# Performance work log

Measured on AMD Instinct MI355X. Metric: run time of the kernel, lower is better.

## Reference

```python
import jax, jax.numpy as jnp
import numpy as np

K = 6

def _diag_indices(H, W):
    # stable argsort of anti-diagonal index i+j over row-major flattening
    i = np.arange(H)[:, None]
    j = np.arange(W)[None, :]
    order = np.argsort((i + j).ravel(), kind='stable')
    return order, np.argsort(order, kind='stable')

def _selective_scan(u, delta, A, Bs, Cs, D, delta_bias):
    # u, delta: (B,K,D,L); A: (K,D,N); Bs,Cs: (B,K,N,L); D,delta_bias: (K,D)
    delta = jax.nn.softplus(delta + delta_bias[None, :, :, None])
    dA = jnp.exp(jnp.einsum('bkdl,kdn->lbkdn', delta, A))          # (L,B,K,D,N)
    dBu = jnp.einsum('bkdl,bknl,bkdl->lbkdn', delta, Bs, u)         # (L,B,K,D,N)
    Cl = jnp.moveaxis(Cs, -1, 0)                                    # (L,B,K,N)
    x0 = jnp.zeros(dA.shape[1:], dA.dtype)
    def step(x, inp):
        dA_t, dBu_t, C_t = inp
        x = dA_t * x + dBu_t
        y = jnp.einsum('bkdn,bkn->bkd', x, C_t)
        return x, y
    _, ys = jax.lax.scan(step, x0, (dA, dBu, Cl))
    y = jnp.moveaxis(ys, 0, -1)                                     # (B,K,D,L)
    return y + u * D[None, :, :, None]

def reference(x, W_in, conv_w, conv_b, x_proj_w, dt_w, dt_b, A_logs, Ds, ln_g, ln_b, W_out):
    B, H, W, C = x.shape
    L = H * W
    di = dt_w.shape[1]
    dt_rank = dt_w.shape[2]
    N = A_logs.shape[1]
    # in_proj (no bias) and split
    xz = jnp.einsum('bhwc,oc->bhwo', x, W_in)
    xx, z = jnp.split(xz, 2, axis=-1)
    # depthwise conv 3x3, SAME padding, + bias, SiLU
    xc = jnp.transpose(xx, (0, 3, 1, 2))                            # (B,di,H,W)
    xc = jax.lax.conv_general_dilated(xc, conv_w, (1, 1), 'SAME',
            feature_group_count=di, dimension_numbers=('NCHW', 'OIHW', 'NCHW'))
    xc = jax.nn.silu(xc + conv_b[None, :, None, None])
    # build 6 scan orderings
    x_flat = xc.reshape(B, di, L)
    x_t = jnp.transpose(xc, (0, 1, 3, 2)).reshape(B, di, L)
    x_hwwh = jnp.stack([x_flat, x_t], axis=1)                       # (B,2,di,L)
    xs4 = jnp.concatenate([x_hwwh, x_hwwh[..., ::-1]], axis=1)      # (B,4,di,L)
    x_invhh = jnp.flip(xc, axis=-1).reshape(B, di, L)               # flip W only
    x_hh = jnp.stack([x_flat, x_invhh], axis=1)                     # (B,2,di,L)
    diag_idx, rev_idx = _diag_indices(H, W)
    xs = jnp.concatenate([xs4, x_hh[..., diag_idx]], axis=1)        # (B,6,di,L)
    # projections
    x_dbl = jnp.einsum('bkdl,kcd->bkcl', xs, x_proj_w)
    dts, Bs, Cs = jnp.split(x_dbl, [dt_rank, dt_rank + N], axis=2)
    dts = jnp.einsum('bkrl,kdr->bkdl', dts, dt_w)
    A = -jnp.exp(A_logs).reshape(K, di, N)
    out_y = _selective_scan(xs, dts, A, Bs, Cs, Ds.reshape(K, di), dt_b)
    # undo the 6 orderings
    inv_y = out_y[:, 2:4][..., ::-1]
    wh_y = jnp.transpose(out_y[:, 1].reshape(B, di, W, H), (0, 1, 3, 2)).reshape(B, di, L)
    invwh_y = jnp.transpose(inv_y[:, 1].reshape(B, di, W, H), (0, 1, 3, 2)).reshape(B, di, L)
    transhh = out_y[:, 4:6][..., rev_idx]
    invhh = transhh[:, 1][..., ::-1]
    y = out_y[:, 0] + inv_y[:, 0] + wh_y + invwh_y + transhh[:, 0] + invhh  # (B,di,L)
    y = jnp.transpose(y, (0, 2, 1)).reshape(B, H, W, di)
    # LayerNorm (eps=1e-5)
    mu = y.mean(-1, keepdims=True)
    var = ((y - mu) ** 2).mean(-1, keepdims=True)
    y = (y - mu) * jax.lax.rsqrt(var + 1e-5) * ln_g + ln_b
    y = y * jax.nn.silu(z)
    return jnp.einsum('bhwd,od->bhwo', y, W_out)

def setup_inputs():
    key = jax.random.key(0)
    ks = jax.random.split(key, 8)
    d_model, di, N, dt_rank = 64, 128, 16, 4
    x = jax.random.normal(ks[0], (1, 64, 64, d_model), jnp.float32)
    W_in = jax.random.normal(ks[1], (2 * di, d_model), jnp.float32) * d_model ** -0.5
    conv_w = jax.random.normal(ks[2], (di, 1, 3, 3), jnp.float32) / 3.0
    conv_b = jnp.zeros((di,), jnp.float32)
    x_proj_w = jax.random.normal(ks[3], (K, dt_rank + 2 * N, di), jnp.float32) * di ** -0.5
    s = dt_rank ** -0.5
    dt_w = jax.random.uniform(ks[4], (K, di, dt_rank), jnp.float32, -s, s)
    dt = jnp.exp(jax.random.uniform(ks[5], (K, di), jnp.float32)
                 * (np.log(0.1) - np.log(0.001)) + np.log(0.001))
    dt = jnp.clip(dt, 1e-4)
    dt_b = dt + jnp.log(-jnp.expm1(-dt))
    A_logs = jnp.log(jnp.tile(jnp.arange(1, N + 1, dtype=jnp.float32)[None, :], (K * di, 1)))
    Ds = jnp.ones((K * di,), jnp.float32)
    ln_g = jnp.ones((di,), jnp.float32)
    ln_b = jnp.zeros((di,), jnp.float32)
    W_out = jax.random.normal(ks[6], (d_model, di), jnp.float32) * di ** -0.5
    return {"x": x, "W_in": W_in, "conv_w": conv_w, "conv_b": conv_b,
            "x_proj_w": x_proj_w, "dt_w": dt_w, "dt_b": dt_b, "A_logs": A_logs,
            "Ds": Ds, "ln_g": ln_g, "ln_b": ln_b, "W_out": W_out}
```

## Files before the change

kernel.cpp:

```cpp
#include <hip/hip_runtime.h>
#include <math.h>

#define L    4096
#define DI   128
#define NS   16
#define KK   6
#define CM   64
#define NC   256
#define CH   16

__device__ __forceinline__ float softplus_f(float x){
    return x > 20.f ? x : __logf(1.f + __expf(x));
}
__device__ __forceinline__ float silu_f(float x){
    return x / (1.f + __expf(-x));
}

__device__ __forceinline__ int rankp(int p){
    int h = p >> 6, w = p & 63, s = h + w;
    int imin = s > 63 ? s - 63 : 0;
    int off = (s < 64) ? (s*(s+1))/2 : 4096 - ((127-s)*(128-s))/2;
    return off + (h - imin);
}

__device__ __forceinline__ int perm_in(int k, int l, const int* __restrict__ diag){
    switch(k){
        case 0: return l;
        case 1: return ((l&63)<<6) | (l>>6);
        case 2: return (L-1) - l;
        case 3: { int m = (L-1)-l; return ((m&63)<<6) | (m>>6); }
        case 4: return diag[l];
        default: return diag[l] ^ 63;
    }
}

__global__ __launch_bounds__(256) void k_init(const float* __restrict__ W_in,
                                              const float* __restrict__ W_out,
                                              const float* __restrict__ conv_w,
                                              int* __restrict__ diag_idx,
                                              float* __restrict__ WI4,
                                              float* __restrict__ WO4,
                                              float* __restrict__ cwT){
    int t = blockIdx.x*256 + threadIdx.x;
    diag_idx[rankp(t)] = t;
    {
        int d4 = t >> 8, o = t & 255;
        ((float4*)WI4)[d4*256 + o] = make_float4(
            W_in[(size_t)o*CM + d4*4+0], W_in[(size_t)o*CM + d4*4+1],
            W_in[(size_t)o*CM + d4*4+2], W_in[(size_t)o*CM + d4*4+3]);
    }
    if(t < 2048){
        int d4 = t >> 6, o = t & 63;
        ((float4*)WO4)[d4*64 + o] = make_float4(
            W_out[(size_t)o*DI + d4*4+0], W_out[(size_t)o*DI + d4*4+1],
            W_out[(size_t)o*DI + d4*4+2], W_out[(size_t)o*DI + d4*4+3]);
    }
    if(t < 9*DI){
        int tap = t >> 7, d = t & 127;
        cwT[t] = conv_w[d*9 + tap];
    }
}

__global__ __launch_bounds__(256) void k_inproj(const float* __restrict__ x,
                                                const float* __restrict__ WI4,
                                                float* __restrict__ xx_t,
                                                float* __restrict__ sz){
    int pb = blockIdx.x * 8;
    int o  = threadIdx.x;
    __shared__ float xr[8][CM];
    if(o < 128) ((float4*)&xr[0][0])[o] = ((const float4*)(x + (size_t)pb*CM))[o];
    float4 w[16];
    const float4* W4 = (const float4*)WI4;
    #pragma unroll
    for(int q=0;q<16;q++) w[q] = W4[q*256 + o];
    __syncthreads();
    float acc[8];
    #pragma unroll
    for(int pi=0;pi<8;pi++) acc[pi] = 0.f;
    #pragma unroll
    for(int q=0;q<16;q++){
        float4 wv = w[q];
        #pragma unroll
        for(int pi=0;pi<8;pi++){
            float4 xv = *((const float4*)&xr[pi][q*4]);
            acc[pi] += wv.x*xv.x + wv.y*xv.y + wv.z*xv.z + wv.w*xv.w;
        }
    }
    #pragma unroll
    for(int pi=0;pi<8;pi++){
        int p = pb + pi;
        if(o < DI) xx_t[(size_t)p*DI + o] = acc[pi];
        else       sz[(size_t)p*DI + (o-DI)] = silu_f(acc[pi]);
    }
}

__global__ __launch_bounds__(256) void k_conv(const float* __restrict__ xx_t,
                                              const float* __restrict__ cwT,
                                              const float* __restrict__ cb,
                                              float* __restrict__ xc_t){
    int idx = blockIdx.x*256 + threadIdx.x;
    int dq = (idx & 31)*4, p = idx >> 5;
    int h = p >> 6, w = p & 63;
    float4 acc = *((const float4*)(cb + dq));
    #pragma unroll
    for(int dh=-1; dh<=1; dh++){
        int hh = h+dh; if(hh < 0 || hh >= 64) continue;
        #pragma unroll
        for(int dw=-1; dw<=1; dw++){
            int ww = w+dw; if(ww < 0 || ww >= 64) continue;
            int tap = (dh+1)*3 + (dw+1);
            float4 xv = *((const float4*)(xx_t + (size_t)(hh*64+ww)*DI + dq));
            float4 wv = *((const float4*)(cwT + tap*DI + dq));
            acc.x += wv.x*xv.x; acc.y += wv.y*xv.y;
            acc.z += wv.z*xv.z; acc.w += wv.w*xv.w;
        }
    }
    *((float4*)(xc_t + (size_t)p*DI + dq)) =
        make_float4(silu_f(acc.x), silu_f(acc.y), silu_f(acc.z), silu_f(acc.w));
}

#define XT_S 132
__global__ __launch_bounds__(128) void k_projscan(const float* __restrict__ xc_t,
                                                  const float* __restrict__ xpw,
                                                  const int* __restrict__ diag,
                                                  const float* __restrict__ dtw,
                                                  const float* __restrict__ dtb,
                                                  const float* __restrict__ A_logs,
                                                  float* __restrict__ dts,
                                                  float* __restrict__ BT,
                                                  float* __restrict__ CT,
                                                  float* __restrict__ apb,
                                                  float* __restrict__ xlb){
    int b = blockIdx.x;
    int k = b >> 7, tile = b & 127;
    int l0 = tile * 32;
    int t = threadIdx.x;
    __shared__ float xt[32*XT_S];
    __shared__ float Btl[32*NS];
    __shared__ float dtt[4*32];

    #pragma unroll
    for(int q=0;q<8;q++){
        int lin = q*128 + t;
        int row = lin >> 5, col4 = lin & 31;
        int p = perm_in(k, l0+row, diag);
        float4 v = ((const float4*)(xc_t + (size_t)p*DI))[col4];
        *((float4*)(xt + row*XT_S + col4*4)) = v;
    }
    __syncthreads();

    {
        int l = t & 31, c0 = (t>>5)*9;
        const float* xr = xt + l*XT_S;
        float acc[9];
        #pragma unroll
        for(int j=0;j<9;j++) acc[j] = 0.f;
        const float4* wbase = (const float4*)(xpw + (size_t)k*36*DI);
        for(int dd4=0; dd4<32; dd4++){
            float4 xv = *((const float4*)(xr + dd4*4));
            #pragma unroll
            for(int j=0;j<9;j++){
                float4 wv = wbase[(c0+j)*32 + dd4];
                acc[j] += wv.x*xv.x + wv.y*xv.y + wv.z*xv.z + wv.w*xv.w;
            }
        }
        #pragma unroll
        for(int j=0;j<9;j++){
            int c = c0 + j;
            if(c < 4){
                dts[((size_t)k*4 + c)*L + l0 + l] = acc[j];
                dtt[c*32 + l] = acc[j];
            } else if(c < 20){
                BT[((size_t)k*L + l0 + l)*NS + (c-4)] = acc[j];
                Btl[l*NS + (c-4)] = acc[j];
            } else {
                CT[((size_t)k*L + l0 + l)*NS + (c-20)] = acc[j];
            }
        }
    }
    __syncthreads();

    int d = t;
    float4 w4 = ((const float4*)dtw)[(size_t)k*DI + d];
    float  bb = dtb[k*DI + d];
    float A[NS];
    {
        const float4* ar = (const float4*)(A_logs + ((size_t)k*DI + d)*NS);
        #pragma unroll
        for(int q=0;q<4;q++){
            float4 a4 = ar[q];
            A[q*4+0] = -__expf(a4.x); A[q*4+1] = -__expf(a4.y);
            A[q*4+2] = -__expf(a4.z); A[q*4+3] = -__expf(a4.w);
        }
    }
    for(int q=0;q<2;q++){
        float xs[NS], ap[NS];
        #pragma unroll
        for(int n=0;n<NS;n++){ xs[n] = 0.f; ap[n] = 1.f; }
        #pragma unroll
        for(int i=0;i<CH;i++){
            int l = q*CH + i;
            float u = xt[l*XT_S + d];
            float dv = bb + w4.x*dtt[l] + w4.y*dtt[32+l] + w4.z*dtt[64+l] + w4.w*dtt[96+l];
            float delta = softplus_f(dv);
            float du = delta*u;
            const float* Bi = Btl + l*NS;
            #pragma unroll
            for(int n=0;n<NS;n++){
                float da = __expf(delta*A[n]);
                xs[n] = da*xs[n] + du*Bi[n];
                ap[n] *= da;
            }
        }
        int bk = k*NC + tile*2 + q;
        float* apd = apb + ((size_t)bk*DI + d)*NS;
        float* xld = xlb + ((size_t)bk*DI + d)*NS;
        #pragma unroll
        for(int qq=0;qq<4;qq++){
            ((float4*)apd)[qq] = make_float4(ap[qq*4],ap[qq*4+1],ap[qq*4+2],ap[qq*4+3]);
            ((float4*)xld)[qq] = make_float4(xs[qq*4],xs[qq*4+1],xs[qq*4+2],xs[qq*4+3]);
        }
    }
}

__global__ __launch_bounds__(512) void k_comb(float* __restrict__ apb,
                                              const float* __restrict__ xlb){
    int k    = blockIdx.x >> 5;
    int gidx = blockIdx.x & 31;
    int seg  = threadIdx.x >> 6;
    int c    = threadIdx.x & 63;
    int rem  = gidx*64 + c;
    size_t sb = (size_t)k*NC*2048 + (size_t)seg*32*2048 + rem;
    float a[32], xl[32];
    #pragma unroll
    for(int j=0;j<32;j++){
        a[j]  = apb[sb + (size_t)j*2048];
        xl[j] = xlb[sb + (size_t)j*2048];
    }
    float Aag = 1.f, Xag = 0.f;
    #pragma unroll
    for(int j=0;j<32;j++){ Xag = a[j]*Xag + xl[j]; Aag *= a[j]; }
    __shared__ float sA[64][8], sX[64][8];
    sA[c][seg] = Aag; sX[c][seg] = Xag;
    __syncthreads();
    if(threadIdx.x < 64){
        float run = 0.f;
        #pragma unroll
        for(int s=0;s<8;s++){
            float at = sA[c][s], xt = sX[c][s];
            sX[c][s] = run;
            run = at*run + xt;
        }
    }
    __syncthreads();
    float run = sX[c][seg];
    #pragma unroll
    for(int j=0;j<32;j++){
        apb[sb + (size_t)j*2048] = run;
        run = a[j]*run + xl[j];
    }
}

__global__ __launch_bounds__(128) void k_scan2(const float* __restrict__ xc_t,
                                               const float* __restrict__ dts,
                                               const float* __restrict__ BT,
                                               const float* __restrict__ CT,
                                               const float* __restrict__ dtw,
                                               const float* __restrict__ dtb,
                                               const float* __restrict__ A_logs,
                                               const float* __restrict__ Dsv,
                                               const int* __restrict__ diag,
                                               const float* __restrict__ inib,
                                               float* __restrict__ yk){
    int bk = blockIdx.x;
    int k = bk >> 8, cc = bk & (NC-1);
    int d = threadIdx.x;
    int l0 = cc*CH;
    __shared__ float Bt[CH*NS];
    __shared__ float Ct[CH*NS];
    __shared__ float dtt[4*CH];
    __shared__ int   pt[CH];
    if(d < 64){
        ((float4*)Bt)[d] = ((const float4*)(BT + ((size_t)k*L + l0)*NS))[d];
        int r = d>>4, i = d&15;
        dtt[d] = dts[((size_t)k*4 + r)*L + l0 + i];
    } else {
        ((float4*)Ct)[d-64] = ((const float4*)(CT + ((size_t)k*L + l0)*NS))[d-64];
    }
    if(d < CH) pt[d] = perm_in(k, l0+d, diag);
    __syncthreads();
    float u[CH];
    #pragma unroll
    for(int i=0;i<CH;i++) u[i] = xc_t[(size_t)pt[i]*DI + d];
    float4 w4 = ((const float4*)dtw)[(size_t)k*DI + d];
    float  bb = dtb[k*DI + d];
    float  Dv = Dsv[k*DI + d];
    float A[NS];
    {
        const float4* ar = (const float4*)(A_logs + ((size_t)k*DI + d)*NS);
        #pragma unroll
        for(int q=0;q<4;q++){
            float4 a4 = ar[q];
            A[q*4+0] = -__expf(a4.x); A[q*4+1] = -__expf(a4.y);
            A[q*4+2] = -__expf(a4.z); A[q*4+3] = -__expf(a4.w);
        }
    }
    float xv[NS];
    {
        const float4* ir = (const float4*)(inib + ((size_t)bk*DI + d)*NS);
        #pragma unroll
        for(int q=0;q<4;q++){
            float4 v = ir[q];
            xv[q*4+0]=v.x; xv[q*4+1]=v.y; xv[q*4+2]=v.z; xv[q*4+3]=v.w;
        }
    }
    #pragma unroll
    for(int i=0;i<CH;i++){
        float dv = bb + w4.x*dtt[i] + w4.y*dtt[CH+i] + w4.z*dtt[2*CH+i] + w4.w*dtt[3*CH+i];
        float delta = softplus_f(dv);
        float du = delta*u[i];
        const float* Bi = Bt + i*NS;
        const float* Ci = Ct + i*NS;
        float y = 0.f;
        #pragma unroll
        for(int n=0;n<NS;n++){
            float da = __expf(delta*A[n]);
            xv[n] = da*xv[n] + du*Bi[n];
            y += xv[n]*Ci[n];
        }
        yk[((size_t)k*L + l0 + i)*DI + d] = y + u[i]*Dv;
    }
}

__global__ __launch_bounds__(128) void k_out(const float* __restrict__ yk,
                                             const float* __restrict__ sz,
                                             const float* __restrict__ ln_g,
                                             const float* __restrict__ ln_b,
                                             const float* __restrict__ WO4,
                                             float* __restrict__ out){
    int pb = blockIdx.x*4;
    int d = threadIdx.x;
    __shared__ float ms[4][DI];
    __shared__ float red[4][2][2];
    float g = ln_g[d], bc = ln_b[d];
    float yv[4];
    #pragma unroll
    for(int pi=0;pi<4;pi++){
        int p = pb+pi;
        int tp = ((p&63)<<6) | (p>>6);
        float y;
        y  = yk[((size_t)0*L + p)*DI + d];
        y += yk[((size_t)1*L + tp)*DI + d];
        y += yk[((size_t)2*L + (L-1-p))*DI + d];
        y += yk[((size_t)3*L + (L-1-tp))*DI + d];
        y += yk[((size_t)4*L + rankp(p))*DI + d];
        y += yk[((size_t)5*L + rankp(L-1-p))*DI + d];
        yv[pi] = y;
        float s1 = y, s2 = y*y;
        #pragma unroll
        for(int m=1;m<64;m<<=1){ s1 += __shfl_xor(s1,m,64); s2 += __shfl_xor(s2,m,64); }
        if((d&63)==0){ red[pi][d>>6][0] = s1; red[pi][d>>6][1] = s2; }
    }
    __syncthreads();
    #pragma unroll
    for(int pi=0;pi<4;pi++){
        float mu  = (red[pi][0][0]+red[pi][1][0]) * (1.f/DI);
        float var = (red[pi][0][1]+red[pi][1][1]) * (1.f/DI) - mu*mu;
        float yh = (yv[pi]-mu)*rsqrtf(var+1e-5f)*g + bc;
        ms[pi][d] = yh * sz[(size_t)(pb+pi)*DI + d];
    }
    __syncthreads();
    int o = d & 63, w = d >> 6;
    const float4* W4 = (const float4*)WO4;
    float acc[2];
    acc[0] = 0.f; acc[1] = 0.f;
    #pragma unroll 8
    for(int d4=0; d4<32; d4++){
        float4 wv = W4[d4*64 + o];
        #pragma unroll
        for(int q=0;q<2;q++){
            float4 xv = *((const float4*)&ms[w*2+q][d4*4]);
            acc[q] += wv.x*xv.x + wv.y*xv.y + wv.z*xv.z + wv.w*xv.w;
        }
    }
    #pragma unroll
    for(int q=0;q<2;q++)
        out[(size_t)(pb + w*2 + q)*CM + o] = acc[q];
}

extern "C" void kernel_launch(void* const* d_in, const int* in_sizes, int n_in,
                              void* d_out, int out_size, void* d_ws, size_t ws_size,
                              hipStream_t stream) {
    const float* x      = (const float*)d_in[0];
    const float* W_in   = (const float*)d_in[1];
    const float* conv_w = (const float*)d_in[2];
    const float* conv_b = (const float*)d_in[3];
    const float* xpw    = (const float*)d_in[4];
    const float* dtw    = (const float*)d_in[5];
    const float* dtb    = (const float*)d_in[6];
    const float* A_logs = (const float*)d_in[7];
    const float* Dsv    = (const float*)d_in[8];
    const float* ln_g   = (const float*)d_in[9];
    const float* ln_b   = (const float*)d_in[10];
    const float* W_out  = (const float*)d_in[11];
    float* out = (float*)d_out;

    float* ws = (float*)d_ws;
    float* xx_t = ws;
    float* sz   = xx_t + (size_t)L*DI;
    float* xc_t = sz   + (size_t)L*DI;
    float* dts  = xc_t + (size_t)L*DI;
    float* BT   = dts  + (size_t)KK*4*L;
    float* CT   = BT   + (size_t)KK*L*NS;
    float* apb  = CT   + (size_t)KK*L*NS;
    float* xlb  = apb  + (size_t)KK*NC*DI*NS;
    float* yk   = xlb  + (size_t)KK*NC*DI*NS;
    int*   diag = (int*)(yk + (size_t)KK*L*DI);
    float* WI4  = (float*)(diag + L);
    float* WO4  = WI4 + (size_t)16*256*4;
    float* cwT  = WO4 + (size_t)32*64*4;

    k_init    <<<L/256, 256, 0, stream>>>(W_in, W_out, conv_w, diag, WI4, WO4, cwT);
    k_inproj  <<<L/8, 256, 0, stream>>>(x, WI4, xx_t, sz);
    k_conv    <<<(L*DI/4)/256, 256, 0, stream>>>(xx_t, cwT, conv_b, xc_t);
    k_projscan<<<KK*128, 128, 0, stream>>>(xc_t, xpw, diag, dtw, dtb, A_logs,
                                           dts, BT, CT, apb, xlb);
    k_comb    <<<KK*32, 512, 0, stream>>>(apb, xlb);
    k_scan2   <<<KK*NC, 128, 0, stream>>>(xc_t, dts, BT, CT, dtw, dtb, A_logs, Dsv, diag, apb, yk);
    k_out     <<<L/4, 128, 0, stream>>>(yk, sz, ln_g, ln_b, WO4, out);
}
```

Baseline: 182.1 us.

## Double projscan block threads, split chunk scans across halves, pad x_proj weights

k_projscan now runs 256 threads per block. Each half of the block scans one of the two 16-step chunks in parallel instead of one thread looping over both. The x_proj weights are repacked in k_init into a zero-padded 40-row layout so that 8 warps each compute 5 output channels. The block index is also remapped to interleave the K directions across adjacent blocks. This targets longer per-thread serial work and low occupancy, at the cost of more threads and some wasted padded-row compute.

```diff
diff --git a/kernel.cpp b/kernel.cpp
--- a/kernel.cpp
+++ b/kernel.cpp
@@ -37,10 +37,12 @@
 __global__ __launch_bounds__(256) void k_init(const float* __restrict__ W_in,
                                               const float* __restrict__ W_out,
                                               const float* __restrict__ conv_w,
+                                              const float* __restrict__ xpw,
                                               int* __restrict__ diag_idx,
                                               float* __restrict__ WI4,
                                               float* __restrict__ WO4,
-                                              float* __restrict__ cwT){
+                                              float* __restrict__ cwT,
+                                              float* __restrict__ PW40){
     int t = blockIdx.x*256 + threadIdx.x;
     diag_idx[rankp(t)] = t;
     {
@@ -58,6 +60,13 @@
     if(t < 9*DI){
         int tap = t >> 7, d = t & 127;
         cwT[t] = conv_w[d*9 + tap];
+    }
+    for(int r = t; r < KK*40*32; r += 4096){
+        int k = r / (40*32), rem = r % (40*32);
+        int c = rem >> 5, dd4 = rem & 31;
+        float4 v = make_float4(0.f, 0.f, 0.f, 0.f);
+        if(c < 36) v = ((const float4*)(xpw + ((size_t)k*36 + c)*DI))[dd4];
+        ((float4*)PW40)[r] = v;
     }
 }
 
@@ -120,8 +129,8 @@
 }
 
 #define XT_S 132
-__global__ __launch_bounds__(128) void k_projscan(const float* __restrict__ xc_t,
-                                                  const float* __restrict__ xpw,
+__global__ __launch_bounds__(256) void k_projscan(const float* __restrict__ xc_t,
+                                                  const float* __restrict__ PW40,
                                                   const int* __restrict__ diag,
                                                   const float* __restrict__ dtw,
                                                   const float* __restrict__ dtb,
@@ -132,7 +141,7 @@
                                                   float* __restrict__ apb,
                                                   float* __restrict__ xlb){
     int b = blockIdx.x;
-    int k = b >> 7, tile = b & 127;
+    int k = b % KK, tile = b / KK;
     int l0 = tile * 32;
     int t = threadIdx.x;
     __shared__ float xt[32*XT_S];
@@ -140,8 +149,8 @@
     __shared__ float dtt[4*32];
 
     #pragma unroll
-    for(int q=0;q<8;q++){
-        int lin = q*128 + t;
+    for(int q=0;q<4;q++){
+        int lin = q*256 + t;
         int row = lin >> 5, col4 = lin & 31;
         int p = perm_in(k, l0+row, diag);
         float4 v = ((const float4*)(xc_t + (size_t)p*DI))[col4];
@@ -150,37 +159,38 @@
     __syncthreads();
 
     {
-        int l = t & 31, c0 = (t>>5)*9;
+        int l = t & 31, g = t >> 5;
         const float* xr = xt + l*XT_S;
-        float acc[9];
-        #pragma unroll
-        for(int j=0;j<9;j++) acc[j] = 0.f;
-        const float4* wbase = (const float4*)(xpw + (size_t)k*36*DI);
+        float acc[5];
+        #pragma unroll
+        for(int j=0;j<5;j++) acc[j] = 0.f;
+        const float4* wbase = (const float4*)PW40 + (size_t)k*40*32;
         for(int dd4=0; dd4<32; dd4++){
             float4 xv = *((const float4*)(xr + dd4*4));
             #pragma unroll
-            for(int j=0;j<9;j++){
-                float4 wv = wbase[(c0+j)*32 + dd4];
+            for(int j=0;j<5;j++){
+                float4 wv = wbase[(g*5+j)*32 + dd4];
                 acc[j] += wv.x*xv.x + wv.y*xv.y + wv.z*xv.z + wv.w*xv.w;
             }
         }
         #pragma unroll
-        for(int j=0;j<9;j++){
-            int c = c0 + j;
+        for(int j=0;j<5;j++){
+            int c = g*5 + j;
             if(c < 4){
                 dts[((size_t)k*4 + c)*L + l0 + l] = acc[j];
                 dtt[c*32 + l] = acc[j];
             } else if(c < 20){
                 BT[((size_t)k*L + l0 + l)*NS + (c-4)] = acc[j];
                 Btl[l*NS + (c-4)] = acc[j];
-            } else {
+            } else if(c < 36){
                 CT[((size_t)k*L + l0 + l)*NS + (c-20)] = acc[j];
             }
         }
     }
     __syncthreads();
 
-    int d = t;
+    int h = t >> 7, d = t & 127;
+    int cc = tile*2 + h;
     float4 w4 = ((const float4*)dtw)[(size_t)k*DI + d];
     float  bb = dtb[k*DI + d];
     float A[NS];
@@ -193,33 +203,31 @@
             A[q*4+2] = -__expf(a4.z); A[q*4+3] = -__expf(a4.w);
         }
     }
-    for(int q=0;q<2;q++){
-        float xs[NS], ap[NS];
-        #pragma unroll
-        for(int n=0;n<NS;n++){ xs[n] = 0.f; ap[n] = 1.f; }
-        #pragma unroll
-        for(int i=0;i<CH;i++){
-            int l = q*CH + i;
-            float u = xt[l*XT_S + d];
-            float dv = bb + w4.x*dtt[l] + w4.y*dtt[32+l] + w4.z*dtt[64+l] + w4.w*dtt[96+l];
-            float delta = softplus_f(dv);
-            float du = delta*u;
-            const float* Bi = Btl + l*NS;
-            #pragma unroll
-            for(int n=0;n<NS;n++){
-                float da = __expf(delta*A[n]);
-                xs[n] = da*xs[n] + du*Bi[n];
-                ap[n] *= da;
-            }
-        }
-        int bk = k*NC + tile*2 + q;
-        float* apd = apb + ((size_t)bk*DI + d)*NS;
-        float* xld = xlb + ((size_t)bk*DI + d)*NS;
-        #pragma unroll
-        for(int qq=0;qq<4;qq++){
-            ((float4*)apd)[qq] = make_float4(ap[qq*4],ap[qq*4+1],ap[qq*4+2],ap[qq*4+3]);
-            ((float4*)xld)[qq] = make_float4(xs[qq*4],xs[qq*4+1],xs[qq*4+2],xs[qq*4+3]);
-        }
+    float xs[NS], ap[NS];
+    #pragma unroll
+    for(int n=0;n<NS;n++){ xs[n] = 0.f; ap[n] = 1.f; }
+    #pragma unroll
+    for(int i=0;i<CH;i++){
+        int l = h*CH + i;
+        float u = xt[l*XT_S + d];
+        float dv = bb + w4.x*dtt[l] + w4.y*dtt[32+l] + w4.z*dtt[64+l] + w4.w*dtt[96+l];
+        float delta = softplus_f(dv);
+        float du = delta*u;
+        const float* Bi = Btl + l*NS;
+        #pragma unroll
+        for(int n=0;n<NS;n++){
+            float da = __expf(delta*A[n]);
+            xs[n] = da*xs[n] + du*Bi[n];
+            ap[n] *= da;
+        }
+    }
+    int bk = k*NC + cc;
+    float* apd = apb + ((size_t)bk*DI + d)*NS;
+    float* xld = xlb + ((size_t)bk*DI + d)*NS;
+    #pragma unroll
+    for(int q=0;q<4;q++){
+        ((float4*)apd)[q] = make_float4(ap[q*4],ap[q*4+1],ap[q*4+2],ap[q*4+3]);
+        ((float4*)xld)[q] = make_float4(xs[q*4],xs[q*4+1],xs[q*4+2],xs[q*4+3]);
     }
 }
 
@@ -419,11 +427,12 @@
     float* WI4  = (float*)(diag + L);
     float* WO4  = WI4 + (size_t)16*256*4;
     float* cwT  = WO4 + (size_t)32*64*4;
-
-    k_init    <<<L/256, 256, 0, stream>>>(W_in, W_out, conv_w, diag, WI4, WO4, cwT);
+    float* PW40 = cwT + (size_t)9*DI;
+
+    k_init    <<<L/256, 256, 0, stream>>>(W_in, W_out, conv_w, xpw, diag, WI4, WO4, cwT, PW40);
     k_inproj  <<<L/8, 256, 0, stream>>>(x, WI4, xx_t, sz);
     k_conv    <<<(L*DI/4)/256, 256, 0, stream>>>(xx_t, cwT, conv_b, xc_t);
-    k_projscan<<<KK*128, 128, 0, stream>>>(xc_t, xpw, diag, dtw, dtb, A_logs,
+    k_projscan<<<KK*128, 256, 0, stream>>>(xc_t, PW40, diag, dtw, dtb, A_logs,
                                            dts, BT, CT, apb, xlb);
     k_comb    <<<KK*32, 512, 0, stream>>>(apb, xlb);
     k_scan2   <<<KK*NC, 128, 0, stream>>>(xc_t, dts, BT, CT, dtw, dtb, A_logs, Dsv, diag, apb, yk);
```

New measurement: 165.3 us (median of 2 runs). 9.3% less time.
